# Performance work log

Measured on AMD Instinct MI355X. Metric: run time of the kernel, lower is better.

Reference implementation:

```python
import jax, jax.numpy as jnp
import numpy as np

B, C, W, H = 8192, 512, 14, 4
D = C // H  # head dim = 128


def setup_inputs() -> dict:
    key = jax.random.key(0)
    ks = jax.random.split(key, 8)
    s = 1.0 / np.sqrt(C).astype(np.float32)
    return {
        "x": jax.random.normal(ks[0], (B, C, W), jnp.float32),
        "Wq": jax.random.normal(ks[1], (C, C), jnp.float32) * s,
        "bq": jax.random.normal(ks[2], (C,), jnp.float32) * 0.01,
        "Wk": jax.random.normal(ks[3], (C, C), jnp.float32) * s,
        "bk": jax.random.normal(ks[4], (C,), jnp.float32) * 0.01,
        "Wv": jax.random.normal(ks[5], (C, C), jnp.float32) * s,
        "bv": jax.random.normal(ks[6], (C,), jnp.float32) * 0.01,
        "rel_w": jax.random.normal(ks[7], (1, H, D, W), jnp.float32),
    }


def reference(x, Wq, bq, Wk, bk, Wv, bv, rel_w):
    # Conv1d(kernel_size=1) == channel-wise linear: out[b,o,w] = sum_c Wm[o,c]*x[b,c,w] + bm[o]
    def proj(Wm, bm):
        y = jnp.einsum('oc,bcw->bow', Wm, x) + bm[None, :, None]
        return y.reshape(B, H, D, W)

    q = proj(Wq, bq)  # [B,H,D,W]
    k = proj(Wk, bk)
    v = proj(Wv, bv)

    # content-content: q^T k over head dim -> [B,H,W,W]
    cc = jnp.einsum('bhdi,bhdj->bhij', q, k)
    # content-position: rel_w^T q -> [B,H,W,W] (rows = relative position, cols = query pos)
    cp = jnp.einsum('hdi,bhdj->bhij', rel_w[0], q)

    attn = jax.nn.softmax(cc + cp, axis=-1)  # softmax over last dim, as in the original

    # out = v @ attn^T : out[b,h,d,i] = sum_j v[b,h,d,j] * attn[b,h,i,j]
    out = jnp.einsum('bhdj,bhij->bhdi', v, attn)
    return out.reshape(B, C, W)
```

## Files before the change

kernel.cpp:

```cpp
#include <hip/hip_runtime.h>
#include <hip/hip_bf16.h>

typedef __bf16 bf16x8 __attribute__((ext_vector_type(8)));
typedef float f32x4 __attribute__((ext_vector_type(4)));
typedef int i32x4 __attribute__((ext_vector_type(4)));

typedef __attribute__((address_space(1))) const void GVoid;
typedef __attribute__((address_space(3))) void LVoid;

#define SX1 16.0f
#define SX1I 0.0625f
#define SX2 4000.0f
#define SW1 400.0f
#define SW1I 0.0025f
#define SW2 100000.0f
#define SR1 32.0f
#define SR1I 0.03125f
#define SR2 8000.0f
#define SC_QK 1.5625e-4f
#define SC_CP 1.953125e-3f
#define CORR 0.004f

static __device__ __forceinline__ float b2f(unsigned short u) {
    union { float f; unsigned int i; } x; x.i = ((unsigned int)u) << 16; return x.f;
}
static __device__ __forceinline__ unsigned short f2b(float f) {
    union { float f; unsigned int u; } x; x.f = f;
    unsigned int r = x.u + 0x7FFFu + ((x.u >> 16) & 1u);
    return (unsigned short)(r >> 16);
}
static __device__ __forceinline__ int q8v(float v, float s) {
    int i = __float2int_rn(v * s);
    return (i > 127) ? 127 : (i < -127 ? -127 : i);
}

__global__ __launch_bounds__(256) void k_prep(const float* __restrict__ Wq, const float* __restrict__ Wk,
                                              const float* __restrict__ Wv, const float* __restrict__ bq,
                                              const float* __restrict__ bk, const float* __restrict__ bv,
                                              const float* __restrict__ relw, char* __restrict__ Wi8,
                                              float* __restrict__ biasA) {
    int o = blockIdx.x;
    int tid = threadIdx.x;
    if (o < 1024) {
        const float* src = (o < 512) ? (Wq + (long)o * 512) : (Wk + (long)(o - 512) * 512);
        char* row = Wi8 + (long)o * 1024;
        for (int c = tid; c < 512; c += 256) {
            float w = src[c];
            int wh = q8v(w, SW1);
            float res = w - (float)wh * SW1I;
            int wl = q8v(res, SW2);
            row[c] = (char)wh;
            row[512 + c] = (char)wl;
        }
    } else if (o < 1536) {
        const float* src = Wv + (long)(o - 1024) * 512;
        char* row = Wi8 + (long)(1152 + (o - 1024)) * 1024;
        for (int c = tid; c < 512; c += 256) {
            float w = src[c];
            int wh = q8v(w, SW1);
            float res = w - (float)wh * SW1I;
            int wl = q8v(res, SW2);
            row[c] = (char)wh;
            row[512 + c] = (char)wl;
        }
    } else if (o < 1592) {
        int t = o - 1536, h = t / 14, i = t - h * 14;
        char* row = Wi8 + (long)(1024 + t) * 1024;
#pragma unroll
        for (int cc = 0; cc < 2; ++cc) {
            int c = tid + cc * 256;
            float acc = 0.f;
            for (int d = 0; d < 128; ++d)
                acc += relw[h * 1792 + d * 14 + i] * Wq[(long)(h * 128 + d) * 512 + c];
            int rh = q8v(acc, SR1);
            float res = acc - (float)rh * SR1I;
            int rl = q8v(res, SR2);
            row[c] = (char)rh;
            row[512 + c] = (char)rl;
        }
        if (tid == 0) {
            float acc = 0.f;
            for (int d = 0; d < 128; ++d) acc += relw[h * 1792 + d * 14 + i] * bq[h * 128 + d];
            biasA[1024 + t] = acc;
        }
    } else {
        for (int i = tid; i < 1664; i += 256) {
            if (i >= 1024 && i < 1080) continue;
            biasA[i] = (i < 512) ? bq[i] : (i < 1024) ? bk[i - 512] : (i < 1152) ? 0.f : bv[i - 1152];
        }
        int* z = (int*)(Wi8 + (long)1080 * 1024);
        for (int idx = tid; idx < 72 * 256; idx += 256) z[idx] = 0;
    }
}

__global__ __launch_bounds__(256) void k_transpose(const float* __restrict__ x,
                                                   char* __restrict__ Ai8, int b0) {
    __shared__ float xl[512 * 15];
    const float* xb = x + (long)(b0 + blockIdx.x) * 7168;
    const float4* xb4 = (const float4*)xb;
    int tid = threadIdx.x;
#pragma unroll
    for (int it = 0; it < 7; ++it) {
        int f = tid + it * 256;
        float4 v = xb4[f];
        float vals[4] = {v.x, v.y, v.z, v.w};
        int e = f * 4;
#pragma unroll
        for (int j = 0; j < 4; ++j) {
            int ee = e + j;
            int c = (ee * 9363) >> 17;
            int w = ee - c * 14;
            xl[c * 15 + w] = vals[j];
        }
    }
    __syncthreads();
    char* irow = Ai8 + (long)blockIdx.x * 14336;
#pragma unroll
    for (int it = 0; it < 7; ++it) {
        int p = tid + it * 256;
        int w = p >> 7, c0 = (p & 127) * 4;
        unsigned int hp = 0, lp = 0;
#pragma unroll
        for (int j = 0; j < 4; ++j) {
            float v = xl[(c0 + j) * 15 + w];
            int xh = q8v(v, SX1);
            float res = v - (float)xh * SX1I;
            int xlo = q8v(res, SX2);
            hp |= ((unsigned int)(xh & 255)) << (8 * j);
            lp |= ((unsigned int)(xlo & 255)) << (8 * j);
        }
        *(unsigned int*)(irow + (long)w * 1024 + c0) = hp;
        *(unsigned int*)(irow + (long)w * 1024 + 512 + c0) = lp;
    }
}

__global__ __launch_bounds__(512, 2) void k_gemmA(const char* __restrict__ Ai8,
                                                  const char* __restrict__ Wi8,
                                                  const float* __restrict__ biasA,
                                                  float* __restrict__ qkf,
                                                  unsigned short* __restrict__ vb, int Mtiles) {
    __shared__ __align__(16) char Ls[2][4][128 * 128];
    int nwg = Mtiles * 13;
    int p = blockIdx.x;
    int xcd = p & 7, o8 = p >> 3;
    int q8_ = nwg >> 3, r8 = nwg & 7;
    int t = (xcd < r8 ? xcd * (q8_ + 1) : r8 * (q8_ + 1) + (xcd - r8) * q8_) + o8;
    int mt = t / 13, nt = t - mt * 13;
    long m0 = (long)mt * 128;
    int n0 = nt * 128;
    int tid = threadIdx.x, lane = tid & 63, wv = tid >> 6;
    int wm = wv >> 1, wn = wv & 1;

    i32x4 accM[2][4], accC[2][4];
#pragma unroll
    for (int i = 0; i < 2; ++i)
#pragma unroll
        for (int j = 0; j < 4; ++j) { accM[i][j] = (i32x4){0, 0, 0, 0}; accC[i][j] = (i32x4){0, 0, 0, 0}; }

#define STAGE(KT, BUF)                                                                           \
    {                                                                                            \
        int kof = (KT) * 128;                                                                    \
        _Pragma("unroll") for (int i = 0; i < 2; ++i) {                                          \
            int row = i * 64 + (tid >> 3);                                                       \
            int gu = (((tid & 7) ^ (row & 7)) << 4);                                             \
            long ao = ((m0 + row) << 10) + kof + gu;                                             \
            long bo = ((long)(n0 + row) << 10) + kof + gu;                                       \
            int dof = i * 8192 + tid * 16;                                                       \
            __builtin_amdgcn_global_load_lds((GVoid*)(Ai8 + ao), (LVoid*)(&Ls[BUF][0][0] + dof), 16, 0, 0); \
            __builtin_amdgcn_global_load_lds((GVoid*)(Ai8 + ao + 512), (LVoid*)(&Ls[BUF][1][0] + dof), 16, 0, 0); \
            __builtin_amdgcn_global_load_lds((GVoid*)(Wi8 + bo), (LVoid*)(&Ls[BUF][2][0] + dof), 16, 0, 0); \
            __builtin_amdgcn_global_load_lds((GVoid*)(Wi8 + bo + 512), (LVoid*)(&Ls[BUF][3][0] + dof), 16, 0, 0); \
        }                                                                                        \
    }

    STAGE(0, 0);
    int cur = 0;
    for (int kt = 0; kt < 4; ++kt) {
        if (kt < 3) {
            if (cur == 0) STAGE(kt + 1, 1) else STAGE(kt + 1, 0);
            asm volatile("s_waitcnt vmcnt(8)" ::: "memory");
        } else {
            asm volatile("s_waitcnt vmcnt(0)" ::: "memory");
        }
        __builtin_amdgcn_s_barrier();
        __builtin_amdgcn_sched_barrier(0);

        const char* Ah = &Ls[cur][0][0];
        const char* Al = &Ls[cur][1][0];
        const char* Bh = &Ls[cur][2][0];
        const char* Bl = &Ls[cur][3][0];
#pragma unroll
        for (int kk = 0; kk < 2; ++kk) {
            i32x4 ah[2], al[2], bh[4], bl[4];
            int kb = kk * 64 + ((lane >> 4) << 4);
#pragma unroll
            for (int mf = 0; mf < 2; ++mf) {
                int row = wm * 32 + mf * 16 + (lane & 15);
                int off = row * 128 + (kb ^ ((row & 7) << 4));
                ah[mf] = *(const i32x4*)(Ah + off);
                al[mf] = *(const i32x4*)(Al + off);
            }
#pragma unroll
            for (int nf = 0; nf < 4; ++nf) {
                int row = wn * 64 + nf * 16 + (lane & 15);
                int off = row * 128 + (kb ^ ((row & 7) << 4));
                bh[nf] = *(const i32x4*)(Bh + off);
                bl[nf] = *(const i32x4*)(Bl + off);
            }
#pragma unroll
            for (int mf = 0; mf < 2; ++mf)
#pragma unroll
                for (int nf = 0; nf < 4; ++nf) {
                    accM[mf][nf] = __builtin_amdgcn_mfma_i32_16x16x64_i8(ah[mf], bh[nf], accM[mf][nf], 0, 0, 0);
                    accC[mf][nf] = __builtin_amdgcn_mfma_i32_16x16x64_i8(ah[mf], bl[nf], accC[mf][nf], 0, 0, 0);
                    accC[mf][nf] = __builtin_amdgcn_mfma_i32_16x16x64_i8(al[mf], bh[nf], accC[mf][nf], 0, 0, 0);
                }
        }
        __builtin_amdgcn_sched_barrier(0);
        __builtin_amdgcn_s_barrier();
        cur ^= 1;
    }
#undef STAGE

#pragma unroll
    for (int nf = 0; nf < 4; ++nf) {
        int n = n0 + wn * 64 + nf * 16 + (lane & 15);
        float scale = (n < 1024) ? SC_QK : (n < 1152 ? SC_CP : SC_QK);
        float bb = biasA[n];
#pragma unroll
        for (int mf = 0; mf < 2; ++mf) {
            long mg = m0 + wm * 32 + mf * 16 + ((lane >> 4) << 2);
#pragma unroll
            for (int r = 0; r < 4; ++r) {
                float val = ((float)accM[mf][nf][r] + CORR * (float)accC[mf][nf][r]) * scale + bb;
                if (n < 1080) qkf[(mg + r) * 1152 + n] = val;
                else if (n >= 1152) vb[(mg + r) * 512 + (n - 1152)] = f2b(val);
            }
        }
    }
}

__global__ __launch_bounds__(512) void k_attn(const float* __restrict__ qkf,
                                              const unsigned short* __restrict__ vb,
                                              float* __restrict__ out, int b0) {
    __shared__ float qs[14 * 512];
    __shared__ float ks[14 * 512];
    __shared__ float cps[56 * 16];
    __shared__ float sl[56 * 16];
    __shared__ unsigned short vs[14 * 512];
    int tid = threadIdx.x;
    long mb = (long)blockIdx.x * 14;
    const float4* qk4 = (const float4*)qkf;
#pragma unroll
    for (int it = 0; it < 7; ++it) {
        int idx = tid + it * 512;
        int w = idx >> 8, c4 = idx & 255;
        float4 v = qk4[(mb + w) * 288 + c4];
        if (c4 < 128) *(float4*)&qs[w * 512 + ((c4 ^ (w & 7)) << 2)] = v;
        else {
            int uu = c4 - 128;
            *(float4*)&ks[w * 512 + ((uu ^ (w & 7)) << 2)] = v;
        }
    }
#pragma unroll
    for (int it = 0; it < 2; ++it) {
        int idx = tid + it * 512;
        if (idx < 784) {
            int w = idx / 56, tt = idx - w * 56;
            cps[tt * 16 + w] = qkf[(mb + w) * 1152 + 1024 + tt];
        }
    }
#pragma unroll
    for (int it = 0; it < 2; ++it) {
        int idx = tid + it * 512;
        if (idx < 896) {
            int w = idx >> 6, uu = idx & 63;
            *(uint4*)&vs[w * 512 + uu * 8] = *(const uint4*)&vb[(mb + w) * 512 + uu * 8];
        }
    }
    __syncthreads();
    if (tid < 196) {
        int h = tid / 49, r = tid - h * 49;
        int i0 = (r / 7) * 2, j0 = (r - (r / 7) * 7) * 2;
        float a00 = 0.f, a01 = 0.f, a10 = 0.f, a11 = 0.f;
#pragma unroll
        for (int d4 = 0; d4 < 32; ++d4) {
            int uu = h * 32 + d4;
            float4 qa = *(const float4*)&qs[i0 * 512 + ((uu ^ (i0 & 7)) << 2)];
            float4 qb = *(const float4*)&qs[(i0 + 1) * 512 + ((uu ^ ((i0 + 1) & 7)) << 2)];
            float4 ka = *(const float4*)&ks[j0 * 512 + ((uu ^ (j0 & 7)) << 2)];
            float4 kb = *(const float4*)&ks[(j0 + 1) * 512 + ((uu ^ ((j0 + 1) & 7)) << 2)];
            a00 += qa.x * ka.x + qa.y * ka.y + qa.z * ka.z + qa.w * ka.w;
            a01 += qa.x * kb.x + qa.y * kb.y + qa.z * kb.z + qa.w * kb.w;
            a10 += qb.x * ka.x + qb.y * ka.y + qb.z * ka.z + qb.w * ka.w;
            a11 += qb.x * kb.x + qb.y * kb.y + qb.z * kb.z + qb.w * kb.w;
        }
        int base = (h * 14 + i0) * 16 + j0;
        sl[base] = a00 + cps[base];
        sl[base + 1] = a01 + cps[base + 1];
        sl[base + 16] = a10 + cps[base + 16];
        sl[base + 17] = a11 + cps[base + 17];
    }
    __syncthreads();
    if (tid < 56) {
        float* row = &sl[tid * 16];
        float m = row[0];
#pragma unroll
        for (int j = 1; j < 14; ++j) m = fmaxf(m, row[j]);
        float ex[14]; float sum = 0.f;
#pragma unroll
        for (int j = 0; j < 14; ++j) { ex[j] = __expf(row[j] - m); sum += ex[j]; }
        float inv = 1.f / sum;
#pragma unroll
        for (int j = 0; j < 14; ++j) row[j] = ex[j] * inv;
    }
    __syncthreads();
    int c = tid, h = c >> 7;
    float vr[14];
#pragma unroll
    for (int j = 0; j < 14; ++j) vr[j] = b2f(vs[j * 512 + c]);
    float* orow = out + (((long)(b0 + blockIdx.x) * 512 + c) * 14);
    float ob[14];
#pragma unroll
    for (int i = 0; i < 14; ++i) {
        const float* ar = &sl[(h * 14 + i) * 16];
        float a = 0.f;
#pragma unroll
        for (int j = 0; j < 14; ++j) a += vr[j] * ar[j];
        ob[i] = a;
    }
#pragma unroll
    for (int t2 = 0; t2 < 7; ++t2)
        *(float2*)(orow + t2 * 2) = make_float2(ob[2 * t2], ob[2 * t2 + 1]);
}

extern "C" void kernel_launch(void* const* d_in, const int* in_sizes, int n_in,
                              void* d_out, int out_size, void* d_ws, size_t ws_size,
                              hipStream_t stream) {
    const float* x    = (const float*)d_in[0];
    const float* Wq   = (const float*)d_in[1];
    const float* bq   = (const float*)d_in[2];
    const float* Wk   = (const float*)d_in[3];
    const float* bk   = (const float*)d_in[4];
    const float* Wv   = (const float*)d_in[5];
    const float* bv   = (const float*)d_in[6];
    const float* relw = (const float*)d_in[7];
    float* out = (float*)d_out;
    char* ws = (char*)d_ws;

    char*  Wi8   = ws;
    float* biasA = (float*)(ws + 1703936);
    const long WS_DATA = 1712128;

    long avail = (long)ws_size - WS_DATA;
    long nbmax = avail / 93184;
    long NBc = (nbmax / 128) * 128;
    if (NBc > 8192) NBc = 8192;
    if (NBc < 128) NBc = 128;

    char*           Ai8 = ws + WS_DATA;
    float*          qkf = (float*)(Ai8 + NBc * 14336);
    unsigned short* vbw = (unsigned short*)(qkf + NBc * 16128);

    k_prep<<<1593, 256, 0, stream>>>(Wq, Wk, Wv, bq, bk, bv, relw, Wi8, biasA);

    for (int b0 = 0; b0 < 8192; b0 += (int)NBc) {
        int nb = 8192 - b0; if (nb > NBc) nb = (int)NBc;
        int Mtiles = (nb * 14) / 128;
        k_transpose<<<nb, 256, 0, stream>>>(x, Ai8, b0);
        k_gemmA<<<Mtiles * 13, 512, 0, stream>>>(Ai8, Wi8, biasA, qkf, vbw, Mtiles);
        k_attn<<<nb, 512, 0, stream>>>(qkf, vbw, out, b0);
    }
}
```

Baseline: 728.7 us.

## Store Q/K/CP intermediates as int16 and retile GEMM to 4 waves with K=64 stages

The GEMM epilogue now writes the q, k and content-position projections as scaled int16 instead of fp32, halving the intermediate buffer that the attention kernel reads back. The attention kernel dequantizes these on load into shared memory. The GEMM is also retiled: 256 threads, each wave computing a 64x64 tile, with 64-byte K stages over 8 iterations and a new LDS swizzle. The aims are to cut global memory traffic and raise per-wave reuse, at the cost of int16 quantization error on q and k and more register pressure per wave.

```diff
diff --git a/kernel.cpp b/kernel.cpp
--- a/kernel.cpp
+++ b/kernel.cpp
@@ -20,6 +20,10 @@
 #define SC_QK 1.5625e-4f
 #define SC_CP 1.953125e-3f
 #define CORR 0.004f
+#define QKS 4096.0f
+#define QKSI 2.44140625e-4f
+#define CPS 256.0f
+#define CPSI 3.90625e-3f
 
 static __device__ __forceinline__ float b2f(unsigned short u) {
     union { float f; unsigned int i; } x; x.i = ((unsigned int)u) << 16; return x.f;
@@ -32,6 +36,15 @@
 static __device__ __forceinline__ int q8v(float v, float s) {
     int i = __float2int_rn(v * s);
     return (i > 127) ? 127 : (i < -127 ? -127 : i);
+}
+static __device__ __forceinline__ short f2s(float v, float s) {
+    int i = __float2int_rn(v * s);
+    i = (i > 32767) ? 32767 : (i < -32767 ? -32767 : i);
+    return (short)i;
+}
+static __device__ __forceinline__ float s2f(unsigned int pair, int hi, float sc) {
+    short s = hi ? (short)(pair >> 16) : (short)(pair & 0xffffu);
+    return (float)s * sc;
 }
 
 __global__ __launch_bounds__(256) void k_prep(const float* __restrict__ Wq, const float* __restrict__ Wk,
@@ -134,12 +147,12 @@
     }
 }
 
-__global__ __launch_bounds__(512, 2) void k_gemmA(const char* __restrict__ Ai8,
+__global__ __launch_bounds__(256, 2) void k_gemmA(const char* __restrict__ Ai8,
                                                   const char* __restrict__ Wi8,
                                                   const float* __restrict__ biasA,
-                                                  float* __restrict__ qkf,
+                                                  short* __restrict__ qkI,
                                                   unsigned short* __restrict__ vb, int Mtiles) {
-    __shared__ __align__(16) char Ls[2][4][128 * 128];
+    __shared__ __align__(16) char Ls[2][4][128 * 64];
     int nwg = Mtiles * 13;
     int p = blockIdx.x;
     int xcd = p & 7, o8 = p >> 3;
@@ -149,23 +162,23 @@
     long m0 = (long)mt * 128;
     int n0 = nt * 128;
     int tid = threadIdx.x, lane = tid & 63, wv = tid >> 6;
-    int wm = wv >> 1, wn = wv & 1;
-
-    i32x4 accM[2][4], accC[2][4];
-#pragma unroll
-    for (int i = 0; i < 2; ++i)
+    int wr = wv >> 1, wc = wv & 1;
+
+    i32x4 accM[4][4], accC[4][4];
+#pragma unroll
+    for (int i = 0; i < 4; ++i)
 #pragma unroll
         for (int j = 0; j < 4; ++j) { accM[i][j] = (i32x4){0, 0, 0, 0}; accC[i][j] = (i32x4){0, 0, 0, 0}; }
 
 #define STAGE(KT, BUF)                                                                           \
     {                                                                                            \
-        int kof = (KT) * 128;                                                                    \
+        int kof = (KT) * 64;                                                                     \
         _Pragma("unroll") for (int i = 0; i < 2; ++i) {                                          \
-            int row = i * 64 + (tid >> 3);                                                       \
-            int gu = (((tid & 7) ^ (row & 7)) << 4);                                             \
+            int row = i * 64 + (tid >> 2);                                                       \
+            int gu = (((tid & 3) + (row >> 1)) & 3) << 4;                                        \
             long ao = ((m0 + row) << 10) + kof + gu;                                             \
             long bo = ((long)(n0 + row) << 10) + kof + gu;                                       \
-            int dof = i * 8192 + tid * 16;                                                       \
+            int dof = i * 4096 + tid * 16;                                                       \
             __builtin_amdgcn_global_load_lds((GVoid*)(Ai8 + ao), (LVoid*)(&Ls[BUF][0][0] + dof), 16, 0, 0); \
             __builtin_amdgcn_global_load_lds((GVoid*)(Ai8 + ao + 512), (LVoid*)(&Ls[BUF][1][0] + dof), 16, 0, 0); \
             __builtin_amdgcn_global_load_lds((GVoid*)(Wi8 + bo), (LVoid*)(&Ls[BUF][2][0] + dof), 16, 0, 0); \
@@ -175,8 +188,8 @@
 
     STAGE(0, 0);
     int cur = 0;
-    for (int kt = 0; kt < 4; ++kt) {
-        if (kt < 3) {
+    for (int kt = 0; kt < 8; ++kt) {
+        if (kt < 7) {
             if (cur == 0) STAGE(kt + 1, 1) else STAGE(kt + 1, 0);
             asm volatile("s_waitcnt vmcnt(8)" ::: "memory");
         } else {
@@ -189,33 +202,30 @@
         const char* Al = &Ls[cur][1][0];
         const char* Bh = &Ls[cur][2][0];
         const char* Bl = &Ls[cur][3][0];
-#pragma unroll
-        for (int kk = 0; kk < 2; ++kk) {
-            i32x4 ah[2], al[2], bh[4], bl[4];
-            int kb = kk * 64 + ((lane >> 4) << 4);
-#pragma unroll
-            for (int mf = 0; mf < 2; ++mf) {
-                int row = wm * 32 + mf * 16 + (lane & 15);
-                int off = row * 128 + (kb ^ ((row & 7) << 4));
-                ah[mf] = *(const i32x4*)(Ah + off);
-                al[mf] = *(const i32x4*)(Al + off);
+        int U = lane >> 4;
+        i32x4 ah[4], al[4], bh[4], bl[4];
+#pragma unroll
+        for (int mf = 0; mf < 4; ++mf) {
+            int row = wr * 64 + mf * 16 + (lane & 15);
+            int off = row * 64 + (((U - (row >> 1)) & 3) << 4);
+            ah[mf] = *(const i32x4*)(Ah + off);
+            al[mf] = *(const i32x4*)(Al + off);
+        }
+#pragma unroll
+        for (int nf = 0; nf < 4; ++nf) {
+            int row = wc * 64 + nf * 16 + (lane & 15);
+            int off = row * 64 + (((U - (row >> 1)) & 3) << 4);
+            bh[nf] = *(const i32x4*)(Bh + off);
+            bl[nf] = *(const i32x4*)(Bl + off);
+        }
+#pragma unroll
+        for (int mf = 0; mf < 4; ++mf)
+#pragma unroll
+            for (int nf = 0; nf < 4; ++nf) {
+                accM[mf][nf] = __builtin_amdgcn_mfma_i32_16x16x64_i8(ah[mf], bh[nf], accM[mf][nf], 0, 0, 0);
+                accC[mf][nf] = __builtin_amdgcn_mfma_i32_16x16x64_i8(ah[mf], bl[nf], accC[mf][nf], 0, 0, 0);
+                accC[mf][nf] = __builtin_amdgcn_mfma_i32_16x16x64_i8(al[mf], bh[nf], accC[mf][nf], 0, 0, 0);
             }
-#pragma unroll
-            for (int nf = 0; nf < 4; ++nf) {
-                int row = wn * 64 + nf * 16 + (lane & 15);
-                int off = row * 128 + (kb ^ ((row & 7) << 4));
-                bh[nf] = *(const i32x4*)(Bh + off);
-                bl[nf] = *(const i32x4*)(Bl + off);
-            }
-#pragma unroll
-            for (int mf = 0; mf < 2; ++mf)
-#pragma unroll
-                for (int nf = 0; nf < 4; ++nf) {
-                    accM[mf][nf] = __builtin_amdgcn_mfma_i32_16x16x64_i8(ah[mf], bh[nf], accM[mf][nf], 0, 0, 0);
-                    accC[mf][nf] = __builtin_amdgcn_mfma_i32_16x16x64_i8(ah[mf], bl[nf], accC[mf][nf], 0, 0, 0);
-                    accC[mf][nf] = __builtin_amdgcn_mfma_i32_16x16x64_i8(al[mf], bh[nf], accC[mf][nf], 0, 0, 0);
-                }
-        }
         __builtin_amdgcn_sched_barrier(0);
         __builtin_amdgcn_s_barrier();
         cur ^= 1;
@@ -224,23 +234,24 @@
 
 #pragma unroll
     for (int nf = 0; nf < 4; ++nf) {
-        int n = n0 + wn * 64 + nf * 16 + (lane & 15);
+        int n = n0 + wc * 64 + nf * 16 + (lane & 15);
         float scale = (n < 1024) ? SC_QK : (n < 1152 ? SC_CP : SC_QK);
         float bb = biasA[n];
 #pragma unroll
-        for (int mf = 0; mf < 2; ++mf) {
-            long mg = m0 + wm * 32 + mf * 16 + ((lane >> 4) << 2);
+        for (int mf = 0; mf < 4; ++mf) {
+            long mg = m0 + wr * 64 + mf * 16 + ((lane >> 4) << 2);
 #pragma unroll
             for (int r = 0; r < 4; ++r) {
                 float val = ((float)accM[mf][nf][r] + CORR * (float)accC[mf][nf][r]) * scale + bb;
-                if (n < 1080) qkf[(mg + r) * 1152 + n] = val;
+                if (n < 1024)       qkI[(mg + r) * 1152 + n] = f2s(val, QKS);
+                else if (n < 1080)  qkI[(mg + r) * 1152 + n] = f2s(val, CPS);
                 else if (n >= 1152) vb[(mg + r) * 512 + (n - 1152)] = f2b(val);
             }
         }
     }
 }
 
-__global__ __launch_bounds__(512) void k_attn(const float* __restrict__ qkf,
+__global__ __launch_bounds__(512) void k_attn(const short* __restrict__ qkI,
                                               const unsigned short* __restrict__ vb,
                                               float* __restrict__ out, int b0) {
     __shared__ float qs[14 * 512];
@@ -250,16 +261,21 @@
     __shared__ unsigned short vs[14 * 512];
     int tid = threadIdx.x;
     long mb = (long)blockIdx.x * 14;
-    const float4* qk4 = (const float4*)qkf;
-#pragma unroll
-    for (int it = 0; it < 7; ++it) {
+    const uint4* qk16 = (const uint4*)qkI;
+#pragma unroll
+    for (int it = 0; it < 4; ++it) {
         int idx = tid + it * 512;
-        int w = idx >> 8, c4 = idx & 255;
-        float4 v = qk4[(mb + w) * 288 + c4];
-        if (c4 < 128) *(float4*)&qs[w * 512 + ((c4 ^ (w & 7)) << 2)] = v;
-        else {
-            int uu = c4 - 128;
-            *(float4*)&ks[w * 512 + ((uu ^ (w & 7)) << 2)] = v;
+        if (idx < 1792) {
+            int w = idx >> 7, c8 = idx & 127;
+            uint4 raw = qk16[(mb + w) * 144 + c8];
+            float4 f0 = make_float4(s2f(raw.x, 0, QKSI), s2f(raw.x, 1, QKSI),
+                                    s2f(raw.y, 0, QKSI), s2f(raw.y, 1, QKSI));
+            float4 f1 = make_float4(s2f(raw.z, 0, QKSI), s2f(raw.z, 1, QKSI),
+                                    s2f(raw.w, 0, QKSI), s2f(raw.w, 1, QKSI));
+            float* base = (c8 < 64) ? qs : ks;
+            int uu0 = (c8 & 63) * 2;
+            *(float4*)&base[w * 512 + ((uu0 ^ (w & 7)) << 2)] = f0;
+            *(float4*)&base[w * 512 + (((uu0 + 1) ^ (w & 7)) << 2)] = f1;
         }
     }
 #pragma unroll
@@ -267,7 +283,7 @@
         int idx = tid + it * 512;
         if (idx < 784) {
             int w = idx / 56, tt = idx - w * 56;
-            cps[tt * 16 + w] = qkf[(mb + w) * 1152 + 1024 + tt];
+            cps[tt * 16 + w] = (float)qkI[(mb + w) * 1152 + 1024 + tt] * CPSI;
         }
     }
 #pragma unroll
@@ -353,14 +369,14 @@
     const long WS_DATA = 1712128;
 
     long avail = (long)ws_size - WS_DATA;
-    long nbmax = avail / 93184;
+    long nbmax = avail / 60928;
     long NBc = (nbmax / 128) * 128;
     if (NBc > 8192) NBc = 8192;
     if (NBc < 128) NBc = 128;
 
     char*           Ai8 = ws + WS_DATA;
-    float*          qkf = (float*)(Ai8 + NBc * 14336);
-    unsigned short* vbw = (unsigned short*)(qkf + NBc * 16128);
+    short*          qkI = (short*)(Ai8 + NBc * 14336);
+    unsigned short* vbw = (unsigned short*)(qkI + NBc * 16128);
 
     k_prep<<<1593, 256, 0, stream>>>(Wq, Wk, Wv, bq, bk, bv, relw, Wi8, biasA);
 
@@ -368,7 +384,7 @@
         int nb = 8192 - b0; if (nb > NBc) nb = (int)NBc;
         int Mtiles = (nb * 14) / 128;
         k_transpose<<<nb, 256, 0, stream>>>(x, Ai8, b0);
-        k_gemmA<<<Mtiles * 13, 512, 0, stream>>>(Ai8, Wi8, biasA, qkf, vbw, Mtiles);
-        k_attn<<<nb, 512, 0, stream>>>(qkf, vbw, out, b0);
-    }
-}
+        k_gemmA<<<Mtiles * 13, 256, 0, stream>>>(Ai8, Wi8, biasA, qkI, vbw, Mtiles);
+        k_attn<<<nb, 512, 0, stream>>>(qkI, vbw, out, b0);
+    }
+}
```

New measurement: 735.2 us. Within noise of the previous version (+0.9%).
